# Optimization experiments

Hardware: AMD Instinct MI355X
Metric: run time of the kernel (lower is better)

## Reference

```python
import jax, jax.numpy as jnp
import numpy as np

N = 50000          # nodes
E = 1_600_000      # edges (avg degree 32)
F_IN = 48          # node features (df columns 1:-1)
H, C = 8, 8        # conv1: 8 heads x 8 channels
NC = 2             # num_classes
NEG_SLOPE = 0.2    # PyG GATConv default leaky_relu slope


def setup_inputs() -> dict:
    key = jax.random.key(0)
    ks = jax.random.split(key, 9)
    s = 0.1
    return {
        "x": jax.random.normal(ks[0], (N, F_IN), jnp.float32),
        "edge_index": jax.random.randint(ks[1], (2, E), 0, N, dtype=jnp.int64),
        "W1": jax.random.normal(ks[2], (F_IN, H * C), jnp.float32) * s,
        "att_src1": jax.random.normal(ks[3], (H, C), jnp.float32) * s,
        "att_dst1": jax.random.normal(ks[4], (H, C), jnp.float32) * s,
        "b1": jnp.zeros((H * C,), jnp.float32),
        "W2": jax.random.normal(ks[5], (H * C, NC), jnp.float32) * s,
        "att_src2": jax.random.normal(ks[6], (1, NC), jnp.float32) * s,
        "att_dst2": jax.random.normal(ks[7], (1, NC), jnp.float32) * s,
        "b2": jnp.zeros((NC,), jnp.float32),
    }


def _gat_conv(x, src, dst, W, a_src, a_dst, b, heads, out_ch, concat):
    """PyG GATConv: linear -> per-edge leaky_relu attention -> segment softmax
    over destination nodes -> scatter-sum aggregation."""
    n = x.shape[0]
    h = (x @ W).reshape(n, heads, out_ch)               # [N, H, C]
    e_src = (h * a_src).sum(-1)                          # [N, H]
    e_dst = (h * a_dst).sum(-1)                          # [N, H]
    e = jax.nn.leaky_relu(e_src[src] + e_dst[dst], NEG_SLOPE)  # [E, H]
    # numerically stable segment softmax over incoming edges of each dst node
    m = jax.ops.segment_max(e, dst, num_segments=n)      # [N, H]
    ex = jnp.exp(e - m[dst])
    den = jax.ops.segment_sum(ex, dst, num_segments=n)   # [N, H]
    alpha = ex / den[dst]                                # [E, H]
    out = jax.ops.segment_sum(h[src] * alpha[:, :, None], dst, num_segments=n)
    out = out.reshape(n, heads * out_ch) if concat else out.mean(axis=1)
    return out + b


def reference(x, edge_index, W1, att_src1, att_dst1, b1, W2, att_src2, att_dst2, b2):
    n = x.shape[0]
    loop = jnp.arange(n, dtype=edge_index.dtype)  # GATConv add_self_loops=True
    src = jnp.concatenate([edge_index[0], loop])
    dst = jnp.concatenate([edge_index[1], loop])
    h = _gat_conv(x, src, dst, W1, att_src1, att_dst1, b1, H, C, True)
    h = jax.nn.elu(h)
    out = _gat_conv(h, src, dst, W2, att_src2, att_dst2, b2, 1, NC, False)
    return jax.nn.log_softmax(out, axis=1)
```

## Files before the change

### kernel.cpp

```cpp
#include <hip/hip_runtime.h>
#include <hip/hip_bf16.h>
#include <math.h>

#define NN 50000
#define FIN 48
#define HC 64
#define NHEAD 8
#define NCH 8
#define NCLS 2
#define NEG 0.2f
#define LOG2E 1.44269504f

#define NPB 98
#define NBKT 512
#define CAP 4096
#define BCHUNK 4096

__global__ void k_zero(int* p, int n) {
    int i = blockIdx.x * blockDim.x + threadIdx.x;
    if (i < n) p[i] = 0;
}


__global__ void k_bin_h1(const int* __restrict__ ei, int* __restrict__ bcur,
                         int* __restrict__ pairs, int e, int tot, int nbin,
                         const float* __restrict__ x, const float* __restrict__ W1,
                         const float* __restrict__ as1, const float* __restrict__ ad1,
                         __hip_bfloat16* __restrict__ h1b, __hip_bfloat16* __restrict__ es1b,
                         float* __restrict__ ed1, int n) {
    __shared__ int hist[NBKT];
    __shared__ int gbase[NBKT];
    __shared__ float Wl[FIN * HC];
    __shared__ float xs[4][FIN];
    __shared__ float hr[4][HC];
    int t = threadIdx.x;
    if ((int)blockIdx.x < nbin) {
        hist[t] = 0; hist[t + 256] = 0;
        __syncthreads();
        int base = blockIdx.x * BCHUNK;
        int end = min(base + BCHUNK, tot);
        for (int i = base + t; i < end; i += 256) {
            int d = (i < e) ? ei[e + i] : (i - e);
            atomicAdd(&hist[d / NPB], 1);
        }
        __syncthreads();
        for (int u = t; u < NBKT; u += 256) {
            int h = hist[u];
            gbase[u] = h ? atomicAdd(&bcur[u], h) : 0;
        }
        __syncthreads();
        hist[t] = 0; hist[t + 256] = 0;
        __syncthreads();
        for (int i = base + t; i < end; i += 256) {
            int s, d;
            if (i < e) { s = ei[i]; d = ei[e + i]; }
            else       { s = d = i - e; }
            int b = d / NPB;
            int p = gbase[b] + atomicAdd(&hist[b], 1);
            if (p < CAP) pairs[b * CAP + p] = ((d - b * NPB) << 16) | s;
        }
    } else {
        for (int i = t; i < FIN * HC; i += 256) Wl[i] = W1[i];
        int ngroups = (n + 3) >> 2;
        int nl = t >> 6, j = t & 63;
        for (int g = blockIdx.x - nbin; g < ngroups; g += gridDim.x - nbin) {
            int nb = g * 4;
            __syncthreads();
            for (int i = t; i < 4 * FIN; i += 256) {
                int l = i / FIN, k = i % FIN;
                int nd = nb + l;
                xs[l][k] = (nd < n) ? x[nd * FIN + k] : 0.f;
            }
            __syncthreads();
            float acc = 0.f;
            #pragma unroll
            for (int k = 0; k < FIN; ++k) acc += xs[nl][k] * Wl[k * HC + j];
            int nd = nb + nl;
            if (nd < n) h1b[nd * HC + j] = __float2bfloat16(acc);
            hr[nl][j] = acc;
            __syncthreads();
            if (j < 16 && nd < n) {
                int hh = j & 7;
                const float* av = (j < 8) ? as1 : ad1;
                float ev = 0.f;
                #pragma unroll
                for (int c = 0; c < NCH; ++c) ev += hr[nl][hh * NCH + c] * av[hh * NCH + c];
                ev *= LOG2E;
                if (j < 8) es1b[nd * NHEAD + hh] = __float2bfloat16(ev);
                else       ed1[nd * NHEAD + hh] = ev;
            }
        }
    }
}


__global__ void k_bucket_csr(const int* __restrict__ pairs, const int* __restrict__ bcur,
                             int* __restrict__ rowptr, int* __restrict__ degv,
                             int* __restrict__ csr, int n) {
    __shared__ int hist[256];
    int b = blockIdx.x, t = threadIdx.x;
    int lo = b * NPB;
    int nn = min(NPB, n - lo);
    if (nn <= 0) return;
    int base = b * CAP;
    int cnt = min(bcur[b], CAP);
    hist[t] = 0;
    __syncthreads();
    for (int i = t; i < cnt; i += 256) {
        atomicAdd(&hist[pairs[base + i] >> 16], 1);
    }
    __syncthreads();
    int v = hist[t];
    for (int off = 1; off < 256; off <<= 1) {
        int y = (t >= off) ? hist[t - off] : 0;
        __syncthreads();
        hist[t] += y;
        __syncthreads();
    }
    int excl = hist[t] - v;
    if (t < nn) { rowptr[lo + t] = base + excl; degv[lo + t] = v; }
    __syncthreads();
    hist[t] = excl;
    __syncthreads();
    for (int i = t; i < cnt; i += 256) {
        int p = pairs[base + i];
        int pos = atomicAdd(&hist[p >> 16], 1);
        csr[base + pos] = p & 0xFFFF;
    }
}


__global__ void k_agg1(const __hip_bfloat16* __restrict__ h1b, const __hip_bfloat16* __restrict__ es1b,
                       const float* __restrict__ ed1, const int* __restrict__ rowptr,
                       const int* __restrict__ degv, const int* __restrict__ csr,
                       const float* __restrict__ b1,
                       const float* __restrict__ W2, const float* __restrict__ as2,
                       const float* __restrict__ ad2, float4* __restrict__ node2, int n) {
    int wid = (blockIdx.x * blockDim.x + threadIdx.x) >> 6;
    if (wid >= n) return;
    int lane = threadIdx.x & 63;
    int j  = lane >> 3;
    int hw = lane & 7;
    int e4 = lane >> 4;
    int r  = lane & 15;
    int ha = r >> 1;
    int ch0 = (ha << 3) + ((r & 1) << 2);
    int wbase = (e4 << 3) + ha;
    int start = rowptr[wid];
    int cnt = degv[wid];
    float edv = ed1[wid * NHEAD + hw];
    float sumw = 0.f;
    float a0 = 0.f, a1 = 0.f, a2 = 0.f, a3 = 0.f;
    int nbatch = cnt >> 3;

    int rv = csr[start + min(lane, cnt - 1)];

    int sl; float ev; uint2 va, vb;
    if (nbatch > 0) {
        sl = __shfl(rv, j, 64);
        ev = __bfloat162float(es1b[sl * NHEAD + hw]);
        int su0 = __shfl(sl, e4 << 3, 64);
        int su1 = __shfl(sl, (4 + e4) << 3, 64);
        va = *(const uint2*)(h1b + su0 * HC + ch0);
        vb = *(const uint2*)(h1b + su1 * HC + ch0);
        for (int b = 1; b < nbatch; ++b) {
            int sl_n;
            if (b < 8) sl_n = __shfl(rv, (b << 3) + j, 64);
            else       sl_n = csr[start + (b << 3) + j];
            float ev_n = __bfloat162float(es1b[sl_n * NHEAD + hw]);
            int su0n = __shfl(sl_n, e4 << 3, 64);
            int su1n = __shfl(sl_n, (4 + e4) << 3, 64);
            uint2 va_n = *(const uint2*)(h1b + su0n * HC + ch0);
            uint2 vb_n = *(const uint2*)(h1b + su1n * HC + ch0);
            float tt = ev + edv;
            tt = fmaxf(tt, NEG * tt);
            float w = exp2f(tt);
            sumw += w;
            float wj0 = __shfl(w, wbase, 64);
            float wj1 = __shfl(w, wbase + 32, 64);
            a0 += wj0 * __uint_as_float(va.x << 16);
            a1 += wj0 * __uint_as_float(va.x & 0xffff0000u);
            a2 += wj0 * __uint_as_float(va.y << 16);
            a3 += wj0 * __uint_as_float(va.y & 0xffff0000u);
            a0 += wj1 * __uint_as_float(vb.x << 16);
            a1 += wj1 * __uint_as_float(vb.x & 0xffff0000u);
            a2 += wj1 * __uint_as_float(vb.y << 16);
            a3 += wj1 * __uint_as_float(vb.y & 0xffff0000u);
            sl = sl_n; ev = ev_n; va = va_n; vb = vb_n;
        }
        float tt = ev + edv;
        tt = fmaxf(tt, NEG * tt);
        float w = exp2f(tt);
        sumw += w;
        float wj0 = __shfl(w, wbase, 64);
        float wj1 = __shfl(w, wbase + 32, 64);
        a0 += wj0 * __uint_as_float(va.x << 16);
        a1 += wj0 * __uint_as_float(va.x & 0xffff0000u);
        a2 += wj0 * __uint_as_float(va.y << 16);
        a3 += wj0 * __uint_as_float(va.y & 0xffff0000u);
        a0 += wj1 * __uint_as_float(vb.x << 16);
        a1 += wj1 * __uint_as_float(vb.x & 0xffff0000u);
        a2 += wj1 * __uint_as_float(vb.y << 16);
        a3 += wj1 * __uint_as_float(vb.y & 0xffff0000u);
    }
    int i = nbatch << 3;
    if (i < cnt) {
        int idx = min(i + j, cnt - 1);
        int slt = (cnt <= 64) ? __shfl(rv, idx, 64) : csr[start + idx];
        float evt = __bfloat162float(es1b[slt * NHEAD + hw]) + edv;
        evt = fmaxf(evt, NEG * evt);
        float w = (i + j < cnt) ? exp2f(evt) : 0.f;
        sumw += w;
        #pragma unroll
        for (int it = 0; it < 2; ++it) {
            int su   = __shfl(slt, ((it << 2) + e4) << 3, 64);
            float wj = __shfl(w, wbase + (it << 5), 64);
            uint2 v = *(const uint2*)(h1b + su * HC + ch0);
            a0 += wj * __uint_as_float(v.x << 16);
            a1 += wj * __uint_as_float(v.x & 0xffff0000u);
            a2 += wj * __uint_as_float(v.y << 16);
            a3 += wj * __uint_as_float(v.y & 0xffff0000u);
        }
    }
    sumw += __shfl_xor(sumw, 8, 64);
    sumw += __shfl_xor(sumw, 16, 64);
    sumw += __shfl_xor(sumw, 32, 64);
    a0 += __shfl_xor(a0, 16, 64); a0 += __shfl_xor(a0, 32, 64);
    a1 += __shfl_xor(a1, 16, 64); a1 += __shfl_xor(a1, 32, 64);
    a2 += __shfl_xor(a2, 16, 64); a2 += __shfl_xor(a2, 32, 64);
    a3 += __shfl_xor(a3, 16, 64); a3 += __shfl_xor(a3, 32, 64);
    float sden = __shfl(sumw, ha, 64);
    float4 bv = *(const float4*)(b1 + ch0);
    float o0 = a0 / sden + bv.x;
    float o1 = a1 / sden + bv.y;
    float o2 = a2 / sden + bv.z;
    float o3 = a3 / sden + bv.w;
    o0 = o0 > 0.f ? o0 : expm1f(o0);
    o1 = o1 > 0.f ? o1 : expm1f(o1);
    o2 = o2 > 0.f ? o2 : expm1f(o2);
    o3 = o3 > 0.f ? o3 : expm1f(o3);
    float4 w01 = *(const float4*)(W2 + ch0 * 2);
    float4 w23 = *(const float4*)(W2 + ch0 * 2 + 4);
    float p0 = o0 * w01.x + o1 * w01.z + o2 * w23.x + o3 * w23.z;
    float p1 = o0 * w01.y + o1 * w01.w + o2 * w23.y + o3 * w23.w;
    #pragma unroll
    for (int off = 8; off > 0; off >>= 1) {
        p0 += __shfl_xor(p0, off, 64);
        p1 += __shfl_xor(p1, off, 64);
    }
    if (lane == 0) {
        float es2v = (p0 * as2[0] + p1 * as2[1]) * LOG2E;
        float ed2v = (p0 * ad2[0] + p1 * ad2[1]) * LOG2E;
        node2[wid] = make_float4(es2v, p0, p1, ed2v);
    }
}


__global__ void k_agg2(const float4* __restrict__ node2, const int* __restrict__ rowptr,
                       const int* __restrict__ degv, const int* __restrict__ csr,
                       const float* __restrict__ b2, float* __restrict__ out, int n) {
    int lane = threadIdx.x & 63;
    int wid = ((blockIdx.x * blockDim.x + threadIdx.x) >> 6) * 4 + (lane >> 4);
    if (wid >= n) return;
    int l16 = lane & 15;
    int start = rowptr[wid];
    int cnt = degv[wid];
    float edv = ((const float*)node2)[wid * 4 + 3];
    float sw = 0.f, a0 = 0.f, a1 = 0.f;
    for (int i = l16; i < cnt; i += 16) {
        int s = __builtin_nontemporal_load(csr + start + i);
        float4 t = node2[s];
        float val = t.x + edv;
        val = fmaxf(val, NEG * val);
        float w = exp2f(val);
        sw += w;
        a0 += w * t.y;
        a1 += w * t.z;
    }
    #pragma unroll
    for (int off = 8; off > 0; off >>= 1) {
        sw += __shfl_xor(sw, off, 16);
        a0 += __shfl_xor(a0, off, 16);
        a1 += __shfl_xor(a1, off, 16);
    }
    if (l16 == 0) {
        float z0 = a0 / sw + b2[0];
        float z1 = a1 / sw + b2[1];
        float mz = fmaxf(z0, z1);
        float lse = mz + logf(__expf(z0 - mz) + __expf(z1 - mz));
        out[wid * NCLS + 0] = z0 - lse;
        out[wid * NCLS + 1] = z1 - lse;
    }
}


extern "C" void kernel_launch(void* const* d_in, const int* in_sizes, int n_in,
                              void* d_out, int out_size, void* d_ws, size_t ws_size,
                              hipStream_t stream) {
    const float* x   = (const float*)d_in[0];
    const int*   ei  = (const int*)d_in[1];
    const float* W1  = (const float*)d_in[2];
    const float* as1 = (const float*)d_in[3];
    const float* ad1 = (const float*)d_in[4];
    const float* b1  = (const float*)d_in[5];
    const float* W2  = (const float*)d_in[6];
    const float* as2 = (const float*)d_in[7];
    const float* ad2 = (const float*)d_in[8];
    const float* b2  = (const float*)d_in[9];
    float* out = (float*)d_out;

    const int n = in_sizes[0] / FIN;
    const int e = in_sizes[1] / 2;
    const int tot = e + n;

    char* ws = (char*)d_ws;
    size_t off = 0;
    auto alloc = [&](size_t bytes) -> void* {
        void* p = ws + off;
        off += (bytes + 255) & ~(size_t)255;
        return p;
    };
    __hip_bfloat16* h1b  = (__hip_bfloat16*)alloc((size_t)n * HC * 2);
    __hip_bfloat16* es1b = (__hip_bfloat16*)alloc((size_t)n * NHEAD * 2);
    int* pairs   = (int*)alloc((size_t)NBKT * CAP * 4);
    int* csr     = (int*)alloc((size_t)NBKT * CAP * 4);
    float* ed1   = (float*)alloc((size_t)n * NHEAD * 4);
    float4* node2 = (float4*)alloc((size_t)n * 16);
    int* rowptr  = (int*)alloc((size_t)n * 4);
    int* degv    = (int*)alloc((size_t)n * 4);
    int* bcur    = (int*)alloc((size_t)NBKT * 4);

    const int nbin = (tot + BCHUNK - 1) / BCHUNK;

    k_zero<<<(NBKT + 255) / 256, 256, 0, stream>>>(bcur, NBKT);
    k_bin_h1<<<nbin + 1024, 256, 0, stream>>>(ei, bcur, pairs, e, tot, nbin,
                                              x, W1, as1, ad1, h1b, es1b, ed1, n);
    k_bucket_csr<<<NBKT, 256, 0, stream>>>(pairs, bcur, rowptr, degv, csr, n);
    k_agg1<<<(n * 64 + 255) / 256, 256, 0, stream>>>(h1b, es1b, ed1, rowptr, degv, csr,
                                                     b1, W2, as2, ad2, node2, n);
    k_agg2<<<(n * 16 + 255) / 256, 256, 0, stream>>>(node2, rowptr, degv, csr, b2, out, n);
}
```

Before: 108.6 us.

## Single-pass register-held binning and fuse h1 projection with bucket CSR build

The binning kernel now reads each edge once, holding up to 8 packed pairs and their local slot in registers across the global offset reservation, instead of making two passes over the edge list. The chunk size is halved so the 8-per-thread register budget covers it, and launch bounds are added. The node feature projection (x@W1 plus attention logits) moves from the binning kernel into the per-bucket CSR build kernel, so it overlaps with CSR construction rather than with binning. The aim is to halve edge-index reads and rebalance work across launches, at the cost of more bin blocks contending on the global bucket atomics.

```diff
diff --git a/kernel.cpp b/kernel.cpp
--- a/kernel.cpp
+++ b/kernel.cpp
@@ -14,7 +14,7 @@
 #define NPB 98
 #define NBKT 512
 #define CAP 4096
-#define BCHUNK 4096
+#define BCHUNK 2048
 
 __global__ void k_zero(int* p, int n) {
     int i = blockIdx.x * blockDim.x + threadIdx.x;
@@ -22,48 +22,96 @@
 }
 
 
-__global__ void k_bin_h1(const int* __restrict__ ei, int* __restrict__ bcur,
-                         int* __restrict__ pairs, int e, int tot, int nbin,
-                         const float* __restrict__ x, const float* __restrict__ W1,
-                         const float* __restrict__ as1, const float* __restrict__ ad1,
-                         __hip_bfloat16* __restrict__ h1b, __hip_bfloat16* __restrict__ es1b,
-                         float* __restrict__ ed1, int n) {
+__global__ __launch_bounds__(256, 4)
+void k_bin(const int* __restrict__ ei, int* __restrict__ bcur,
+           int* __restrict__ pairs, int e, int tot) {
     __shared__ int hist[NBKT];
     __shared__ int gbase[NBKT];
+    int t = threadIdx.x;
+    hist[t] = 0; hist[t + 256] = 0;
+    __syncthreads();
+    int base = blockIdx.x * BCHUNK;
+    int end = min(base + BCHUNK, tot);
+    int pk[8];
+    int bp[8];
+    #pragma unroll
+    for (int k = 0; k < 8; ++k) {
+        int i = base + t + k * 256;
+        if (i < end) {
+            int s, d;
+            if (i < e) { s = ei[i]; d = ei[e + i]; }
+            else       { s = d = i - e; }
+            int b = d / NPB;
+            int p = atomicAdd(&hist[b], 1);
+            pk[k] = ((d - b * NPB) << 16) | s;
+            bp[k] = (b << 16) | p;
+        } else bp[k] = -1;
+    }
+    __syncthreads();
+    for (int u = t; u < NBKT; u += 256) {
+        int h = hist[u];
+        gbase[u] = h ? atomicAdd(&bcur[u], h) : 0;
+    }
+    __syncthreads();
+    #pragma unroll
+    for (int k = 0; k < 8; ++k) {
+        if (bp[k] >= 0) {
+            int b = bp[k] >> 16;
+            int p = gbase[b] + (bp[k] & 0xFFFF);
+            if (p < CAP) pairs[b * CAP + p] = pk[k];
+        }
+    }
+}
+
+
+__global__ void k_h1csr(const int* __restrict__ pairs, const int* __restrict__ bcur,
+                        int* __restrict__ rowptr, int* __restrict__ degv,
+                        int* __restrict__ csr,
+                        const float* __restrict__ x, const float* __restrict__ W1,
+                        const float* __restrict__ as1, const float* __restrict__ ad1,
+                        __hip_bfloat16* __restrict__ h1b, __hip_bfloat16* __restrict__ es1b,
+                        float* __restrict__ ed1, int n) {
+    __shared__ int hist[256];
     __shared__ float Wl[FIN * HC];
     __shared__ float xs[4][FIN];
     __shared__ float hr[4][HC];
     int t = threadIdx.x;
-    if ((int)blockIdx.x < nbin) {
-        hist[t] = 0; hist[t + 256] = 0;
+    if ((int)blockIdx.x < NBKT) {
+        int b = blockIdx.x;
+        int lo = b * NPB;
+        int nn = min(NPB, n - lo);
+        if (nn <= 0) return;
+        int base = b * CAP;
+        int cnt = min(bcur[b], CAP);
+        hist[t] = 0;
         __syncthreads();
-        int base = blockIdx.x * BCHUNK;
-        int end = min(base + BCHUNK, tot);
-        for (int i = base + t; i < end; i += 256) {
-            int d = (i < e) ? ei[e + i] : (i - e);
-            atomicAdd(&hist[d / NPB], 1);
+        for (int i = t; i < cnt; i += 256) {
+            atomicAdd(&hist[pairs[base + i] >> 16], 1);
         }
         __syncthreads();
-        for (int u = t; u < NBKT; u += 256) {
-            int h = hist[u];
-            gbase[u] = h ? atomicAdd(&bcur[u], h) : 0;
-        }
+        int v = hist[t];
+        for (int off = 1; off < 256; off <<= 1) {
+            int y = (t >= off) ? hist[t - off] : 0;
+            __syncthreads();
+            hist[t] += y;
+            __syncthreads();
+        }
+        int excl = hist[t] - v;
+        if (t < nn) { rowptr[lo + t] = base + excl; degv[lo + t] = v; }
         __syncthreads();
-        hist[t] = 0; hist[t + 256] = 0;
+        hist[t] = excl;
         __syncthreads();
-        for (int i = base + t; i < end; i += 256) {
-            int s, d;
-            if (i < e) { s = ei[i]; d = ei[e + i]; }
-            else       { s = d = i - e; }
-            int b = d / NPB;
-            int p = gbase[b] + atomicAdd(&hist[b], 1);
-            if (p < CAP) pairs[b * CAP + p] = ((d - b * NPB) << 16) | s;
+        for (int i = t; i < cnt; i += 256) {
+            int p = pairs[base + i];
+            int pos = atomicAdd(&hist[p >> 16], 1);
+            csr[base + pos] = p & 0xFFFF;
         }
     } else {
         for (int i = t; i < FIN * HC; i += 256) Wl[i] = W1[i];
         int ngroups = (n + 3) >> 2;
         int nl = t >> 6, j = t & 63;
-        for (int g = blockIdx.x - nbin; g < ngroups; g += gridDim.x - nbin) {
+        int GB = gridDim.x - NBKT;
+        for (int g = blockIdx.x - NBKT; g < ngroups; g += GB) {
             int nb = g * 4;
             __syncthreads();
             for (int i = t; i < 4 * FIN; i += 256) {
@@ -90,42 +138,6 @@
                 else       ed1[nd * NHEAD + hh] = ev;
             }
         }
-    }
-}
-
-
-__global__ void k_bucket_csr(const int* __restrict__ pairs, const int* __restrict__ bcur,
-                             int* __restrict__ rowptr, int* __restrict__ degv,
-                             int* __restrict__ csr, int n) {
-    __shared__ int hist[256];
-    int b = blockIdx.x, t = threadIdx.x;
-    int lo = b * NPB;
-    int nn = min(NPB, n - lo);
-    if (nn <= 0) return;
-    int base = b * CAP;
-    int cnt = min(bcur[b], CAP);
-    hist[t] = 0;
-    __syncthreads();
-    for (int i = t; i < cnt; i += 256) {
-        atomicAdd(&hist[pairs[base + i] >> 16], 1);
-    }
-    __syncthreads();
-    int v = hist[t];
-    for (int off = 1; off < 256; off <<= 1) {
-        int y = (t >= off) ? hist[t - off] : 0;
-        __syncthreads();
-        hist[t] += y;
-        __syncthreads();
-    }
-    int excl = hist[t] - v;
-    if (t < nn) { rowptr[lo + t] = base + excl; degv[lo + t] = v; }
-    __syncthreads();
-    hist[t] = excl;
-    __syncthreads();
-    for (int i = t; i < cnt; i += 256) {
-        int p = pairs[base + i];
-        int pos = atomicAdd(&hist[p >> 16], 1);
-        csr[base + pos] = p & 0xFFFF;
     }
 }
 
@@ -333,9 +345,9 @@
     const int nbin = (tot + BCHUNK - 1) / BCHUNK;
 
     k_zero<<<(NBKT + 255) / 256, 256, 0, stream>>>(bcur, NBKT);
-    k_bin_h1<<<nbin + 1024, 256, 0, stream>>>(ei, bcur, pairs, e, tot, nbin,
-                                              x, W1, as1, ad1, h1b, es1b, ed1, n);
-    k_bucket_csr<<<NBKT, 256, 0, stream>>>(pairs, bcur, rowptr, degv, csr, n);
+    k_bin<<<nbin, 256, 0, stream>>>(ei, bcur, pairs, e, tot);
+    k_h1csr<<<NBKT + 1024, 256, 0, stream>>>(pairs, bcur, rowptr, degv, csr,
+                                             x, W1, as1, ad1, h1b, es1b, ed1, n);
     k_agg1<<<(n * 64 + 255) / 256, 256, 0, stream>>>(h1b, es1b, ed1, rowptr, degv, csr,
                                                      b1, W2, as2, ad2, node2, n);
     k_agg2<<<(n * 16 + 255) / 256, 256, 0, stream>>>(node2, rowptr, degv, csr, b2, out, n);
```

Measured after the change: 117.3 us. +8.0%, slower.
